# Kernel tuning notes

Measured on AMD Instinct MI355X. Metric: run time of the kernel, lower is better.

## Reference

```python
import jax, jax.numpy as jnp
import numpy as np

_CODESZ = 8   # E8 codeword dimension
_OFFSET = 0.25  # half-integer shift applied to D8 points


def _build_grid():
    # Faithful replication of get_grid(): cartesian product of arange(-4,4)
    # over 8 dims (torch.cartesian_prod order == 'ij' meshgrid, last dim fastest),
    # keep points with even coordinate sum and squared norm <= 10 (D8 subset),
    # then concat [d8 - 1/4, d8 + 1/4]. Yields 55650 codewords of dim 8.
    rng = np.arange(-4, 4, dtype=np.int8)
    pts = np.stack(np.meshgrid(*([rng] * _CODESZ), indexing='ij'), axis=-1).reshape(-1, _CODESZ)
    s = pts.sum(axis=-1, dtype=np.int16)
    n2 = (pts.astype(np.int16) * pts).sum(axis=-1)  # max 8*16 fits int16
    d8 = pts[(s % 2 == 0) & (n2 <= 10)].astype(np.float32)  # [27825, 8]
    grid = np.concatenate([d8 - _OFFSET, d8 + _OFFSET], axis=0)  # [55650, 8]
    grid_norm = (grid * grid).sum(axis=-1)  # diag(grid @ grid.T), [55650]
    return jnp.asarray(grid), jnp.asarray(grid_norm)


def setup_inputs() -> dict:
    key = jax.random.key(0)
    X = jax.random.normal(key, (8192, _CODESZ), dtype=jnp.float32)
    grid, grid_norm = _build_grid()
    return {"X": X, "grid": grid, "grid_norm": grid_norm}


def reference(X, grid, grid_norm):
    # quantize(X, return_idx=True):
    # nearest codeword under L2 <=> argmax of 2*X@g - ||g||^2
    scores = 2.0 * (X @ grid.T) - grid_norm          # [N, 55650]
    idx = jnp.argmax(scores, axis=-1)                # [N]
    vals = jnp.take(grid, idx, axis=0)               # [N, 8]
    idx_i16 = (idx + (-2 ** 15)).astype(jnp.int16)   # idx_offset + int16 cast
    return vals, idx_i16
```

## Files before the change

kernel.cpp:

```cpp
#include <hip/hip_runtime.h>
#include <math.h>


typedef short short8 __attribute__((ext_vector_type(8)));
typedef float f32x4  __attribute__((ext_vector_type(4)));

constexpr int NROWS  = 8192;
constexpr int NCW    = 55650;
constexpr int NT16   = 3488;
constexpr int NG     = 436;
constexpr int NCWP2  = NT16 * 16;
constexpr int NCHUNK = 32;
constexpr int RBLK   = 32;

constexpr size_t OFF_GB = 0;
constexpr size_t OFF_XS = OFF_GB + (size_t)NCWP2 * 32;
constexpr size_t OFF_BK = OFF_XS + (size_t)NROWS * 64;

__device__ inline unsigned short bf16_rne(float f) {
  unsigned int u = __float_as_uint(f);
  unsigned int r = u + 0x7FFFu + ((u >> 16) & 1u);
  return (unsigned short)(r >> 16);
}
__device__ inline float bf16_f(unsigned short h) {
  return __uint_as_float(((unsigned int)h) << 16);
}
__device__ inline unsigned int enc_ord(float f) {
  unsigned int u = __float_as_uint(f);
  return (u & 0x80000000u) ? ~u : (u | 0x80000000u);
}
__device__ inline float dec_ord(unsigned int e) {
  unsigned int u = (e & 0x80000000u) ? (e & 0x7FFFFFFFu) : ~e;
  return __uint_as_float(u);
}

__global__ __launch_bounds__(256) void e8_prep(
    const float* __restrict__ X, const float* __restrict__ G,
    const float* __restrict__ GN, unsigned short* __restrict__ Gb,
    unsigned short* __restrict__ Xs, unsigned long long* __restrict__ best) {
  int i = blockIdx.x * 256 + threadIdx.x;
  if (i < NCWP2) {
    unsigned short g16[16];
    if (i < NCW) {
      for (int j = 0; j < 8; ++j) g16[j] = bf16_rne(G[(size_t)i*8+j]);
      g16[8] = bf16_rne(GN[i]);
      for (int j = 9; j < 16; ++j) g16[j] = 0;
    } else {
      for (int j = 0; j < 8; ++j) g16[j] = 0;
      g16[8] = 0x7F7F;
      for (int j = 9; j < 16; ++j) g16[j] = 0;
    }
    uint4* dst = reinterpret_cast<uint4*>(Gb + (size_t)i * 16);
    dst[0] = *reinterpret_cast<uint4*>(&g16[0]);
    dst[1] = *reinterpret_cast<uint4*>(&g16[8]);
  } else if (i < NCWP2 + NROWS) {
    int r = i - NCWP2;
    unsigned short hh[8], mm[8], ll[8], qq[8];
    for (int j = 0; j < 8; ++j) {
      float s = 2.0f * X[(size_t)r*8+j];
      unsigned short h = bf16_rne(s);  float r1 = s  - bf16_f(h);
      unsigned short m = bf16_rne(r1); float r2 = r1 - bf16_f(m);
      unsigned short l = bf16_rne(r2);
      hh[j] = h; mm[j] = m; ll[j] = l;
      qq[j] = (j == 0) ? (unsigned short)0xBF80 : 0;
    }
    uint4* dst = reinterpret_cast<uint4*>(Xs + (size_t)r * 32);
    dst[0] = *reinterpret_cast<uint4*>(hh);
    dst[1] = *reinterpret_cast<uint4*>(mm);
    dst[2] = *reinterpret_cast<uint4*>(ll);
    dst[3] = *reinterpret_cast<uint4*>(qq);
    best[r] = 0ull;
  }
}

#define MV(d, s) "v_mov_b32 v" #d ", v" #s "\n\t"
#define MX(d, s) "v_max_f32 v" #d ", v" #d ", v" #s "\n\t"

#define T16A \
  "s_waitcnt vmcnt(1)\n\t" \
  "v_mfma_f32_16x16x32_bf16 v[72:75],  v[44:47], v[56:59], v[52:55]\n\t" \
  "v_mfma_f32_16x16x32_bf16 v[76:79],  v[44:47], v[60:63], v[52:55]\n\t" \
  "v_mfma_f32_16x16x32_bf16 v[80:83],  v[44:47], v[64:67], v[52:55]\n\t" \
  "v_mfma_f32_16x16x32_bf16 v[84:87],  v[44:47], v[68:71], v[52:55]\n\t" \
  "global_load_dwordx4 v[44:47], v40, %[gb]\n\t" \
  "v_add_u32 v40, 0x200, v40\n\t"

#define T16B \
  "s_waitcnt vmcnt(1)\n\t" \
  "v_mfma_f32_16x16x32_bf16 v[88:91],   v[48:51], v[56:59], v[52:55]\n\t" \
  "v_mfma_f32_16x16x32_bf16 v[92:95],   v[48:51], v[60:63], v[52:55]\n\t" \
  "v_mfma_f32_16x16x32_bf16 v[96:99],   v[48:51], v[64:67], v[52:55]\n\t" \
  "v_mfma_f32_16x16x32_bf16 v[100:103], v[48:51], v[68:71], v[52:55]\n\t" \
  "global_load_dwordx4 v[48:51], v40, %[gb]\n\t" \
  "v_add_u32 v40, 0x200, v40\n\t"

#define MOV16 \
  MV(104,72) MV(105,73) MV(106,74) MV(107,75) MV(108,76) MV(109,77) \
  MV(110,78) MV(111,79) MV(112,80) MV(113,81) MV(114,82) MV(115,83) \
  MV(116,84) MV(117,85) MV(118,86) MV(119,87)

#define MAXA16 \
  MX(104,72) MX(105,73) MX(106,74) MX(107,75) MX(108,76) MX(109,77) \
  MX(110,78) MX(111,79) MX(112,80) MX(113,81) MX(114,82) MX(115,83) \
  MX(116,84) MX(117,85) MX(118,86) MX(119,87)

#define MAXB16 \
  MX(104,88)  MX(105,89)  MX(106,90)  MX(107,91)  MX(108,92)  MX(109,93) \
  MX(110,94)  MX(111,95)  MX(112,96)  MX(113,97)  MX(114,98)  MX(115,99) \
  MX(116,100) MX(117,101) MX(118,102) MX(119,103)

#define TREETRACK \
  MX(104,105) MX(106,107) MX(108,109) MX(110,111) \
  MX(112,113) MX(114,115) MX(116,117) MX(118,119) \
  MX(104,106) MX(108,110) MX(112,114) MX(116,118) \
  "v_cmp_gt_f32 vcc, v104, v120\n\t" \
  "v_cndmask_b32 v124, v124, %[gi], vcc\n\t" \
  "v_max_f32 v120, v120, v104\n\t" \
  "v_cmp_gt_f32 vcc, v108, v121\n\t" \
  "v_cndmask_b32 v125, v125, %[gi], vcc\n\t" \
  "v_max_f32 v121, v121, v108\n\t" \
  "v_cmp_gt_f32 vcc, v112, v122\n\t" \
  "v_cndmask_b32 v126, v126, %[gi], vcc\n\t" \
  "v_max_f32 v122, v122, v112\n\t" \
  "v_cmp_gt_f32 vcc, v116, v123\n\t" \
  "v_cndmask_b32 v127, v127, %[gi], vcc\n\t" \
  "v_max_f32 v123, v123, v116\n\t"

#define GROUP16 \
  T16A T16B MOV16 T16A MAXB16 T16B MAXA16 \
  T16A MAXB16 T16B MAXA16 T16A MAXB16 T16B MAXA16 \
  "s_nop 7\n\t" "s_nop 7\n\t" MAXB16 TREETRACK "s_nop 0"

#define CLOBS \
  "v40","v41","v42","v43","v44","v45","v46","v47","v48","v49", \
  "v50","v51","v52","v53","v54","v55","v56","v57","v58","v59", \
  "v60","v61","v62","v63","v64","v65","v66","v67","v68","v69", \
  "v70","v71","v72","v73","v74","v75","v76","v77","v78","v79", \
  "v80","v81","v82","v83","v84","v85","v86","v87","v88","v89", \
  "v90","v91","v92","v93","v94","v95","v96","v97","v98","v99", \
  "v100","v101","v102","v103","v104","v105","v106","v107","v108","v109", \
  "v110","v111","v112","v113","v114","v115","v116","v117","v118","v119", \
  "v120","v121","v122","v123","v124","v125","v126","v127"

__global__ __launch_bounds__(256, 4) void e8_main(
    const unsigned short* __restrict__ Gb,
    const unsigned short* __restrict__ Xs,
    unsigned long long* __restrict__ best) {
  const int lane = threadIdx.x & 63;
  const int wave = threadIdx.x >> 6;
  const int l15 = lane & 15, kg = lane >> 4;
  const int rowbase = blockIdx.x * 256 + wave * 64;

  const int g0 = blockIdx.y * NG / NCHUNK;
  const int g1 = (blockIdx.y + 1) * NG / NCHUNK;
  const unsigned long long gbv = (unsigned long long)Gb;
  const unsigned long long xsv = (unsigned long long)Xs;

  unsigned avo = (unsigned)g0 * 4096u + (unsigned)l15 * 32u +
                 (kg == 3 ? 16u : 0u);
  unsigned bvo = (unsigned)(rowbase + l15) * 64u + (unsigned)kg * 16u;

  asm volatile(
      "v_mov_b32 v40, %[ao]\n\t"
      "v_mov_b32 v52, 0\n\t" "v_mov_b32 v53, 0\n\t"
      "v_mov_b32 v54, 0\n\t" "v_mov_b32 v55, 0\n\t"
      "v_mov_b32 v120, 0xff800000\n\t" "v_mov_b32 v121, 0xff800000\n\t"
      "v_mov_b32 v122, 0xff800000\n\t" "v_mov_b32 v123, 0xff800000\n\t"
      "v_mov_b32 v124, 0\n\t" "v_mov_b32 v125, 0\n\t"
      "v_mov_b32 v126, 0\n\t" "v_mov_b32 v127, 0\n\t"
      "global_load_dwordx4 v[56:59], %[bo], %[xs]\n\t"
      "global_load_dwordx4 v[60:63], %[bo], %[xs] offset:1024\n\t"
      "global_load_dwordx4 v[64:67], %[bo], %[xs] offset:2048\n\t"
      "global_load_dwordx4 v[68:71], %[bo], %[xs] offset:3072\n\t"
      "global_load_dwordx4 v[44:47], v40, %[gb]\n\t"
      "v_add_u32 v40, 0x200, v40\n\t"
      "global_load_dwordx4 v[48:51], v40, %[gb]\n\t"
      "v_add_u32 v40, 0x200, v40\n\t"
      "s_waitcnt vmcnt(0)"
      :: [gb]"s"(gbv), [xs]"s"(xsv), [ao]"v"(avo), [bo]"v"(bvo)
      : CLOBS, "memory");

  for (int g = g0; g < g1; ++g) {
    asm volatile(GROUP16
        :: [gb]"s"(gbv), [gi]"v"(g)
        : CLOBS, "vcc", "memory");
  }

  float bs0, bs1, bs2, bs3; int bi0, bi1, bi2, bi3;
  asm volatile(
      "s_waitcnt vmcnt(0)\n\t"
      "v_mov_b32 %0, v120\n\t" "v_mov_b32 %1, v121\n\t"
      "v_mov_b32 %2, v122\n\t" "v_mov_b32 %3, v123\n\t"
      "v_mov_b32 %4, v124\n\t" "v_mov_b32 %5, v125\n\t"
      "v_mov_b32 %6, v126\n\t" "v_mov_b32 %7, v127"
      : "=v"(bs0), "=v"(bs1), "=v"(bs2), "=v"(bs3),
        "=v"(bi0), "=v"(bi1), "=v"(bi2), "=v"(bi3) :: "memory");

  const float bsa[4] = {bs0, bs1, bs2, bs3};
  const int   bia[4] = {bi0, bi1, bi2, bi3};
#pragma unroll
  for (int t = 0; t < 4; ++t) {
    unsigned long long key =
        ((unsigned long long)enc_ord(bsa[t]) << 32) | (unsigned int)(~bia[t]);
    unsigned long long o = __shfl_xor(key, 16, 64);
    key = (o > key) ? o : key;
    o = __shfl_xor(key, 32, 64);
    key = (o > key) ? o : key;
    if (lane < 16)
      atomicMax(&best[(size_t)rowbase + t * 16 + l15], key);
  }
}

__global__ __launch_bounds__(256) void e8_resolve(
    const unsigned short* __restrict__ Gb,
    const unsigned short* __restrict__ Xs, const float* __restrict__ G,
    const unsigned long long* __restrict__ best, float* __restrict__ out) {
  const int lane = threadIdx.x & 63;
  const int wave = threadIdx.x >> 6;
  const int l15 = lane & 15, kg = lane >> 4;
  const int rt = blockIdx.x;

  short8 b;
  {
    const size_t row = (size_t)rt * 16 + l15;
    b = *reinterpret_cast<const short8*>(Xs + (row*4 + kg)*8);
  }
  f32x4 cz = {0.f, 0.f, 0.f, 0.f};

  for (int j = wave * 4; j < wave * 4 + 4; ++j) {
    const int srow = rt * 16 + j;
    const unsigned long long k = best[srow];
    const float sstar = dec_ord((unsigned int)(k >> 32));
    const int gwin = (int)(~(unsigned int)(k & 0xFFFFFFFFull));

    const int tb = gwin * 8;
    int cand = 0x7FFFFFFF;
    for (int tt = tb; tt < tb + 8; ++tt) {
      const unsigned short* ga =
          Gb + (size_t)tt * 256 + (size_t)l15 * 16 + (kg == 3 ? 8 : 0);
      short8 a = *reinterpret_cast<const short8*>(ga);
      f32x4 d = __builtin_amdgcn_mfma_f32_16x16x32_bf16(a, b, cz, 0, 0, 0);

      int tc = 0x0FFFFFFF;
#pragma unroll
      for (int r = 3; r >= 0; --r)
        tc = (d[r] == sstar) ? r : tc;
      const int gidx = tt * 16 + kg * 4 + tc;
      cand = (gidx < cand) ? gidx : cand;
    }
    if (l15 != j) cand = 0x7FFFFFFF;
    int o = __shfl_xor(cand, 16, 64); cand = min(cand, o);
    o = __shfl_xor(cand, 32, 64);     cand = min(cand, o);
    if (lane == j) {
      const float4* g = reinterpret_cast<const float4*>(G + (size_t)cand * 8);
      float4 v0 = g[0], v1 = g[1];
      float4* od = reinterpret_cast<float4*>(out + (size_t)srow * 8);
      od[0] = v0; od[1] = v1;
      out[(size_t)NROWS * 8 + srow] = (float)(cand - 32768);
    }
  }
}

extern "C" void kernel_launch(void* const* d_in, const int* in_sizes, int n_in,
                              void* d_out, int out_size, void* d_ws, size_t ws_size,
                              hipStream_t stream) {
  const float* X  = (const float*)d_in[0];
  const float* G  = (const float*)d_in[1];
  const float* GN = (const float*)d_in[2];
  float* out = (float*)d_out;

  char* ws = (char*)d_ws;
  unsigned short*     Gb   = (unsigned short*)(ws + OFF_GB);
  unsigned short*     Xs   = (unsigned short*)(ws + OFF_XS);
  unsigned long long* best = (unsigned long long*)(ws + OFF_BK);

  e8_prep<<<(NCWP2 + NROWS + 255) / 256, 256, 0, stream>>>(X, G, GN, Gb, Xs, best);
  e8_main<<<dim3(RBLK, NCHUNK), 256, 0, stream>>>(Gb, Xs, best);
  e8_resolve<<<512, 256, 0, stream>>>(Gb, Xs, G, best, out);
}
```

Measured before the change: 45.00 us.

## Stage codeword tiles in LDS with double buffering and fp32 norm accumulator init

Codeword tiles are repacked into 320-byte blocks holding 16 bf16 codewords plus their negated fp32 norms. Each group of 8 tiles is staged cooperatively into a double-buffered LDS region and read with ds_read_b128. The negated norm now enters as the MFMA accumulator input instead of an extra bf16 K-lane, so the norm subtraction is done in fp32 rather than bf16. This is meant to cut redundant per-wave global loads and use LDS reuse across the four waves. In exchange it adds a block barrier per group and changes the score rounding used by argmax.

```diff
diff --git a/kernel.cpp b/kernel.cpp
--- a/kernel.cpp
+++ b/kernel.cpp
@@ -4,6 +4,7 @@
 
 typedef short short8 __attribute__((ext_vector_type(8)));
 typedef float f32x4  __attribute__((ext_vector_type(4)));
+typedef unsigned int u32x4 __attribute__((ext_vector_type(4)));
 
 constexpr int NROWS  = 8192;
 constexpr int NCW    = 55650;
@@ -14,7 +15,7 @@
 constexpr int RBLK   = 32;
 
 constexpr size_t OFF_GB = 0;
-constexpr size_t OFF_XS = OFF_GB + (size_t)NCWP2 * 32;
+constexpr size_t OFF_XS = OFF_GB + (size_t)NT16 * 320;
 constexpr size_t OFF_BK = OFF_XS + (size_t)NROWS * 64;
 
 __device__ inline unsigned short bf16_rne(float f) {
@@ -36,23 +37,23 @@
 
 __global__ __launch_bounds__(256) void e8_prep(
     const float* __restrict__ X, const float* __restrict__ G,
-    const float* __restrict__ GN, unsigned short* __restrict__ Gb,
+    const float* __restrict__ GN, unsigned char* __restrict__ GbB,
     unsigned short* __restrict__ Xs, unsigned long long* __restrict__ best) {
   int i = blockIdx.x * 256 + threadIdx.x;
   if (i < NCWP2) {
-    unsigned short g16[16];
+    unsigned char* gt = GbB + (size_t)(i >> 4) * 320;
+    unsigned short c8[8];
+    float cgn;
     if (i < NCW) {
-      for (int j = 0; j < 8; ++j) g16[j] = bf16_rne(G[(size_t)i*8+j]);
-      g16[8] = bf16_rne(GN[i]);
-      for (int j = 9; j < 16; ++j) g16[j] = 0;
+      for (int j = 0; j < 8; ++j) c8[j] = bf16_rne(G[(size_t)i*8+j]);
+      cgn = -GN[i];
     } else {
-      for (int j = 0; j < 8; ++j) g16[j] = 0;
-      g16[8] = 0x7F7F;
-      for (int j = 9; j < 16; ++j) g16[j] = 0;
-    }
-    uint4* dst = reinterpret_cast<uint4*>(Gb + (size_t)i * 16);
-    dst[0] = *reinterpret_cast<uint4*>(&g16[0]);
-    dst[1] = *reinterpret_cast<uint4*>(&g16[8]);
+      for (int j = 0; j < 8; ++j) c8[j] = 0;
+      cgn = -3.0e38f;
+    }
+    *reinterpret_cast<u32x4*>(gt + (size_t)(i & 15) * 16) =
+        *reinterpret_cast<u32x4*>(c8);
+    *reinterpret_cast<float*>(gt + 256 + (size_t)(i & 15) * 4) = cgn;
   } else if (i < NCWP2 + NROWS) {
     int r = i - NCWP2;
     unsigned short hh[8], mm[8], ll[8], qq[8];
@@ -61,14 +62,13 @@
       unsigned short h = bf16_rne(s);  float r1 = s  - bf16_f(h);
       unsigned short m = bf16_rne(r1); float r2 = r1 - bf16_f(m);
       unsigned short l = bf16_rne(r2);
-      hh[j] = h; mm[j] = m; ll[j] = l;
-      qq[j] = (j == 0) ? (unsigned short)0xBF80 : 0;
-    }
-    uint4* dst = reinterpret_cast<uint4*>(Xs + (size_t)r * 32);
-    dst[0] = *reinterpret_cast<uint4*>(hh);
-    dst[1] = *reinterpret_cast<uint4*>(mm);
-    dst[2] = *reinterpret_cast<uint4*>(ll);
-    dst[3] = *reinterpret_cast<uint4*>(qq);
+      hh[j] = h; mm[j] = m; ll[j] = l; qq[j] = 0;
+    }
+    u32x4* dst = reinterpret_cast<u32x4*>(Xs + (size_t)r * 32);
+    dst[0] = *reinterpret_cast<u32x4*>(hh);
+    dst[1] = *reinterpret_cast<u32x4*>(mm);
+    dst[2] = *reinterpret_cast<u32x4*>(ll);
+    dst[3] = *reinterpret_cast<u32x4*>(qq);
     best[r] = 0ull;
   }
 }
@@ -76,62 +76,74 @@
 #define MV(d, s) "v_mov_b32 v" #d ", v" #s "\n\t"
 #define MX(d, s) "v_max_f32 v" #d ", v" #d ", v" #s "\n\t"
 
-#define T16A \
-  "s_waitcnt vmcnt(1)\n\t" \
-  "v_mfma_f32_16x16x32_bf16 v[72:75],  v[44:47], v[56:59], v[52:55]\n\t" \
-  "v_mfma_f32_16x16x32_bf16 v[76:79],  v[44:47], v[60:63], v[52:55]\n\t" \
-  "v_mfma_f32_16x16x32_bf16 v[80:83],  v[44:47], v[64:67], v[52:55]\n\t" \
-  "v_mfma_f32_16x16x32_bf16 v[84:87],  v[44:47], v[68:71], v[52:55]\n\t" \
-  "global_load_dwordx4 v[44:47], v40, %[gb]\n\t" \
-  "v_add_u32 v40, 0x200, v40\n\t"
-
-#define T16B \
-  "s_waitcnt vmcnt(1)\n\t" \
-  "v_mfma_f32_16x16x32_bf16 v[88:91],   v[48:51], v[56:59], v[52:55]\n\t" \
-  "v_mfma_f32_16x16x32_bf16 v[92:95],   v[48:51], v[60:63], v[52:55]\n\t" \
-  "v_mfma_f32_16x16x32_bf16 v[96:99],   v[48:51], v[64:67], v[52:55]\n\t" \
-  "v_mfma_f32_16x16x32_bf16 v[100:103], v[48:51], v[68:71], v[52:55]\n\t" \
-  "global_load_dwordx4 v[48:51], v40, %[gb]\n\t" \
-  "v_add_u32 v40, 0x200, v40\n\t"
+#define TE(P) \
+  "s_waitcnt lgkmcnt(2)\n\t" \
+  "v_mfma_f32_16x16x32_bf16 v[76:79], v[44:47], v[60:63], v[52:55]\n\t" \
+  "v_mfma_f32_16x16x32_bf16 v[80:83], v[44:47], v[64:67], v[52:55]\n\t" \
+  "v_mfma_f32_16x16x32_bf16 v[84:87], v[44:47], v[68:71], v[52:55]\n\t" \
+  "v_mfma_f32_16x16x32_bf16 v[88:91], v[44:47], v[72:75], v[52:55]\n\t" \
+  "ds_read_b128 v[44:47], v40 offset:" P "\n\t" \
+  "ds_read_b128 v[52:55], v41 offset:" P "\n\t"
+
+#define TO(P) \
+  "s_waitcnt lgkmcnt(2)\n\t" \
+  "v_mfma_f32_16x16x32_bf16 v[92:95],   v[48:51], v[60:63], v[56:59]\n\t" \
+  "v_mfma_f32_16x16x32_bf16 v[96:99],   v[48:51], v[64:67], v[56:59]\n\t" \
+  "v_mfma_f32_16x16x32_bf16 v[100:103], v[48:51], v[68:71], v[56:59]\n\t" \
+  "v_mfma_f32_16x16x32_bf16 v[104:107], v[48:51], v[72:75], v[56:59]\n\t" \
+  "ds_read_b128 v[48:51], v40 offset:" P "\n\t" \
+  "ds_read_b128 v[56:59], v41 offset:" P "\n\t"
 
 #define MOV16 \
-  MV(104,72) MV(105,73) MV(106,74) MV(107,75) MV(108,76) MV(109,77) \
-  MV(110,78) MV(111,79) MV(112,80) MV(113,81) MV(114,82) MV(115,83) \
-  MV(116,84) MV(117,85) MV(118,86) MV(119,87)
+  MV(108,76) MV(109,77) MV(110,78) MV(111,79) MV(112,80) MV(113,81) \
+  MV(114,82) MV(115,83) MV(116,84) MV(117,85) MV(118,86) MV(119,87) \
+  MV(120,88) MV(121,89) MV(122,90) MV(123,91)
 
 #define MAXA16 \
-  MX(104,72) MX(105,73) MX(106,74) MX(107,75) MX(108,76) MX(109,77) \
-  MX(110,78) MX(111,79) MX(112,80) MX(113,81) MX(114,82) MX(115,83) \
-  MX(116,84) MX(117,85) MX(118,86) MX(119,87)
+  MX(108,76) MX(109,77) MX(110,78) MX(111,79) MX(112,80) MX(113,81) \
+  MX(114,82) MX(115,83) MX(116,84) MX(117,85) MX(118,86) MX(119,87) \
+  MX(120,88) MX(121,89) MX(122,90) MX(123,91)
 
 #define MAXB16 \
-  MX(104,88)  MX(105,89)  MX(106,90)  MX(107,91)  MX(108,92)  MX(109,93) \
-  MX(110,94)  MX(111,95)  MX(112,96)  MX(113,97)  MX(114,98)  MX(115,99) \
-  MX(116,100) MX(117,101) MX(118,102) MX(119,103)
-
-#define TREETRACK \
-  MX(104,105) MX(106,107) MX(108,109) MX(110,111) \
-  MX(112,113) MX(114,115) MX(116,117) MX(118,119) \
-  MX(104,106) MX(108,110) MX(112,114) MX(116,118) \
-  "v_cmp_gt_f32 vcc, v104, v120\n\t" \
-  "v_cndmask_b32 v124, v124, %[gi], vcc\n\t" \
-  "v_max_f32 v120, v120, v104\n\t" \
-  "v_cmp_gt_f32 vcc, v108, v121\n\t" \
-  "v_cndmask_b32 v125, v125, %[gi], vcc\n\t" \
-  "v_max_f32 v121, v121, v108\n\t" \
-  "v_cmp_gt_f32 vcc, v112, v122\n\t" \
-  "v_cndmask_b32 v126, v126, %[gi], vcc\n\t" \
-  "v_max_f32 v122, v122, v112\n\t" \
-  "v_cmp_gt_f32 vcc, v116, v123\n\t" \
-  "v_cndmask_b32 v127, v127, %[gi], vcc\n\t" \
-  "v_max_f32 v123, v123, v116\n\t"
-
-#define GROUP16 \
-  T16A T16B MOV16 T16A MAXB16 T16B MAXA16 \
-  T16A MAXB16 T16B MAXA16 T16A MAXB16 T16B MAXA16 \
-  "s_nop 7\n\t" "s_nop 7\n\t" MAXB16 TREETRACK "s_nop 0"
+  MX(108,92)  MX(109,93)  MX(110,94)  MX(111,95)  MX(112,96)  MX(113,97) \
+  MX(114,98)  MX(115,99)  MX(116,100) MX(117,101) MX(118,102) MX(119,103) \
+  MX(120,104) MX(121,105) MX(122,106) MX(123,107)
+
+#define TREE \
+  MX(108,109) MX(110,111) MX(112,113) MX(114,115) \
+  MX(116,117) MX(118,119) MX(120,121) MX(122,123) \
+  MX(108,110) MX(112,114) MX(116,118) MX(120,122)
+
+#define TRACK \
+  "v_cmp_gt_f32 vcc, v108, v24\n\t" \
+  "v_cndmask_b32 v28, v28, %[gi], vcc\n\t" \
+  "v_max_f32 v24, v24, v108\n\t" \
+  "v_cmp_gt_f32 vcc, v112, v25\n\t" \
+  "v_cndmask_b32 v29, v29, %[gi], vcc\n\t" \
+  "v_max_f32 v25, v25, v112\n\t" \
+  "v_cmp_gt_f32 vcc, v116, v26\n\t" \
+  "v_cndmask_b32 v30, v30, %[gi], vcc\n\t" \
+  "v_max_f32 v26, v26, v116\n\t" \
+  "v_cmp_gt_f32 vcc, v120, v27\n\t" \
+  "v_cndmask_b32 v31, v31, %[gi], vcc\n\t" \
+  "v_max_f32 v27, v27, v120\n\t"
+
+#define BATCH8 \
+  "v_mov_b32 v40, %[la]\n\t" \
+  "v_mov_b32 v41, %[lc]\n\t" \
+  "ds_read_b128 v[44:47], v40\n\t" \
+  "ds_read_b128 v[52:55], v41\n\t" \
+  "ds_read_b128 v[48:51], v40 offset:320\n\t" \
+  "ds_read_b128 v[56:59], v41 offset:320\n\t" \
+  TE("640") TO("960") MOV16 \
+  TE("1280") MAXB16 TO("1600") MAXA16 \
+  TE("1920") MAXB16 TO("2240") MAXA16 \
+  TE("2560") MAXB16 TO("2880") MAXA16 \
+  "s_nop 7\n\t" "s_nop 7\n\t" \
+  MAXB16 TREE TRACK "s_nop 0"
 
 #define CLOBS \
+  "v24","v25","v26","v27","v28","v29","v30","v31", \
   "v40","v41","v42","v43","v44","v45","v46","v47","v48","v49", \
   "v50","v51","v52","v53","v54","v55","v56","v57","v58","v59", \
   "v60","v61","v62","v63","v64","v65","v66","v67","v68","v69", \
@@ -140,59 +152,87 @@
   "v90","v91","v92","v93","v94","v95","v96","v97","v98","v99", \
   "v100","v101","v102","v103","v104","v105","v106","v107","v108","v109", \
   "v110","v111","v112","v113","v114","v115","v116","v117","v118","v119", \
-  "v120","v121","v122","v123","v124","v125","v126","v127"
+  "v120","v121","v122","v123"
 
 __global__ __launch_bounds__(256, 4) void e8_main(
-    const unsigned short* __restrict__ Gb,
+    const unsigned char* __restrict__ GbB,
     const unsigned short* __restrict__ Xs,
     unsigned long long* __restrict__ best) {
-  const int lane = threadIdx.x & 63;
-  const int wave = threadIdx.x >> 6;
+  const int tid  = threadIdx.x;
+  const int lane = tid & 63;
+  const int wave = tid >> 6;
   const int l15 = lane & 15, kg = lane >> 4;
   const int rowbase = blockIdx.x * 256 + wave * 64;
 
+  __shared__ char smem[6912];
+  ((volatile char*)smem)[tid] = 0;
+
   const int g0 = blockIdx.y * NG / NCHUNK;
   const int g1 = (blockIdx.y + 1) * NG / NCHUNK;
-  const unsigned long long gbv = (unsigned long long)Gb;
   const unsigned long long xsv = (unsigned long long)Xs;
 
-  unsigned avo = (unsigned)g0 * 4096u + (unsigned)l15 * 32u +
-                 (kg == 3 ? 16u : 0u);
-  unsigned bvo = (unsigned)(rowbase + l15) * 64u + (unsigned)kg * 16u;
+  const unsigned bvo = (unsigned)(rowbase + l15) * 64u + (unsigned)kg * 16u;
 
   asm volatile(
-      "v_mov_b32 v40, %[ao]\n\t"
-      "v_mov_b32 v52, 0\n\t" "v_mov_b32 v53, 0\n\t"
-      "v_mov_b32 v54, 0\n\t" "v_mov_b32 v55, 0\n\t"
-      "v_mov_b32 v120, 0xff800000\n\t" "v_mov_b32 v121, 0xff800000\n\t"
-      "v_mov_b32 v122, 0xff800000\n\t" "v_mov_b32 v123, 0xff800000\n\t"
-      "v_mov_b32 v124, 0\n\t" "v_mov_b32 v125, 0\n\t"
-      "v_mov_b32 v126, 0\n\t" "v_mov_b32 v127, 0\n\t"
-      "global_load_dwordx4 v[56:59], %[bo], %[xs]\n\t"
-      "global_load_dwordx4 v[60:63], %[bo], %[xs] offset:1024\n\t"
-      "global_load_dwordx4 v[64:67], %[bo], %[xs] offset:2048\n\t"
-      "global_load_dwordx4 v[68:71], %[bo], %[xs] offset:3072\n\t"
-      "global_load_dwordx4 v[44:47], v40, %[gb]\n\t"
-      "v_add_u32 v40, 0x200, v40\n\t"
-      "global_load_dwordx4 v[48:51], v40, %[gb]\n\t"
-      "v_add_u32 v40, 0x200, v40\n\t"
+      "v_mov_b32 v24, 0xff800000\n\t" "v_mov_b32 v25, 0xff800000\n\t"
+      "v_mov_b32 v26, 0xff800000\n\t" "v_mov_b32 v27, 0xff800000\n\t"
+      "v_mov_b32 v28, 0\n\t" "v_mov_b32 v29, 0\n\t"
+      "v_mov_b32 v30, 0\n\t" "v_mov_b32 v31, 0\n\t"
+      "global_load_dwordx4 v[60:63], %[bo], %[xs]\n\t"
+      "global_load_dwordx4 v[64:67], %[bo], %[xs] offset:1024\n\t"
+      "global_load_dwordx4 v[68:71], %[bo], %[xs] offset:2048\n\t"
+      "global_load_dwordx4 v[72:75], %[bo], %[xs] offset:3072\n\t"
       "s_waitcnt vmcnt(0)"
-      :: [gb]"s"(gbv), [xs]"s"(xsv), [ao]"v"(avo), [bo]"v"(bvo)
+      :: [xs]"s"(xsv), [bo]"v"(bvo)
       : CLOBS, "memory");
 
+  if (tid < 80) {
+    const u32x4* s = reinterpret_cast<const u32x4*>(
+        GbB + (size_t)g0 * 2560 + (size_t)tid * 32);
+    u32x4 a = s[0], b2 = s[1];
+    unsigned doff = (unsigned)tid * 32u;
+    asm volatile(
+        "ds_write_b128 %[ad], %[v0]\n\t"
+        "ds_write_b128 %[ad], %[v1] offset:16"
+        :: [ad]"v"(doff), [v0]"v"(a), [v1]"v"(b2) : "memory");
+  }
+  __syncthreads();
+
   for (int g = g0; g < g1; ++g) {
-    asm volatile(GROUP16
-        :: [gb]"s"(gbv), [gi]"v"(g)
+    const int gnx = g + 1;
+    const bool do_stage = (gnx < g1) && (tid < 80);
+    u32x4 va = {0,0,0,0}, vb2 = {0,0,0,0};
+    if (do_stage) {
+      const u32x4* s = reinterpret_cast<const u32x4*>(
+          GbB + (size_t)gnx * 2560 + (size_t)tid * 32);
+      va = s[0]; vb2 = s[1];
+    }
+
+    const unsigned par = (unsigned)((g - g0) & 1) * 3328u;
+    const unsigned la = par + (unsigned)l15 * 16u;
+    const unsigned lc = par + 256u + (unsigned)kg * 16u;
+    asm volatile(BATCH8
+        :: [la]"v"(la), [lc]"v"(lc), [gi]"v"(g)
         : CLOBS, "vcc", "memory");
+
+    if (do_stage) {
+      const unsigned doff =
+          (unsigned)((gnx - g0) & 1) * 3328u + (unsigned)tid * 32u;
+      asm volatile(
+          "ds_write_b128 %[ad], %[v0]\n\t"
+          "ds_write_b128 %[ad], %[v1] offset:16"
+          :: [ad]"v"(doff), [v0]"v"(va), [v1]"v"(vb2) : "memory");
+    }
+    __syncthreads();
   }
 
   float bs0, bs1, bs2, bs3; int bi0, bi1, bi2, bi3;
   asm volatile(
-      "s_waitcnt vmcnt(0)\n\t"
-      "v_mov_b32 %0, v120\n\t" "v_mov_b32 %1, v121\n\t"
-      "v_mov_b32 %2, v122\n\t" "v_mov_b32 %3, v123\n\t"
-      "v_mov_b32 %4, v124\n\t" "v_mov_b32 %5, v125\n\t"
-      "v_mov_b32 %6, v126\n\t" "v_mov_b32 %7, v127"
+      "s_waitcnt vmcnt(0) lgkmcnt(0)\n\t"
+      "v_mov_b32 %0, v24\n\t" "v_mov_b32 %1, v25\n\t"
+      "v_mov_b32 %2, v26\n\t" "v_mov_b32 %3, v27\n\t"
+      "v_mov_b32 %4, v28\n\t" "v_mov_b32 %5, v29\n\t"
+      "v_mov_b32 %6, v30\n\t" "v_mov_b32 %7, v31"
       : "=v"(bs0), "=v"(bs1), "=v"(bs2), "=v"(bs3),
         "=v"(bi0), "=v"(bi1), "=v"(bi2), "=v"(bi3) :: "memory");
 
@@ -212,7 +252,7 @@
 }
 
 __global__ __launch_bounds__(256) void e8_resolve(
-    const unsigned short* __restrict__ Gb,
+    const unsigned char* __restrict__ GbB,
     const unsigned short* __restrict__ Xs, const float* __restrict__ G,
     const unsigned long long* __restrict__ best, float* __restrict__ out) {
   const int lane = threadIdx.x & 63;
@@ -225,7 +265,6 @@
     const size_t row = (size_t)rt * 16 + l15;
     b = *reinterpret_cast<const short8*>(Xs + (row*4 + kg)*8);
   }
-  f32x4 cz = {0.f, 0.f, 0.f, 0.f};
 
   for (int j = wave * 4; j < wave * 4 + 4; ++j) {
     const int srow = rt * 16 + j;
@@ -236,10 +275,10 @@
     const int tb = gwin * 8;
     int cand = 0x7FFFFFFF;
     for (int tt = tb; tt < tb + 8; ++tt) {
-      const unsigned short* ga =
-          Gb + (size_t)tt * 256 + (size_t)l15 * 16 + (kg == 3 ? 8 : 0);
-      short8 a = *reinterpret_cast<const short8*>(ga);
-      f32x4 d = __builtin_amdgcn_mfma_f32_16x16x32_bf16(a, b, cz, 0, 0, 0);
+      const unsigned char* gt = GbB + (size_t)tt * 320;
+      short8 a = *reinterpret_cast<const short8*>(gt + (size_t)l15 * 16);
+      f32x4 C = *reinterpret_cast<const f32x4*>(gt + 256 + (size_t)kg * 16);
+      f32x4 d = __builtin_amdgcn_mfma_f32_16x16x32_bf16(a, b, C, 0, 0, 0);
 
       int tc = 0x0FFFFFFF;
 #pragma unroll
@@ -270,11 +309,11 @@
   float* out = (float*)d_out;
 
   char* ws = (char*)d_ws;
-  unsigned short*     Gb   = (unsigned short*)(ws + OFF_GB);
+  unsigned char*      GbB  = (unsigned char*)(ws + OFF_GB);
   unsigned short*     Xs   = (unsigned short*)(ws + OFF_XS);
   unsigned long long* best = (unsigned long long*)(ws + OFF_BK);
 
-  e8_prep<<<(NCWP2 + NROWS + 255) / 256, 256, 0, stream>>>(X, G, GN, Gb, Xs, best);
-  e8_main<<<dim3(RBLK, NCHUNK), 256, 0, stream>>>(Gb, Xs, best);
-  e8_resolve<<<512, 256, 0, stream>>>(Gb, Xs, G, best, out);
-}
+  e8_prep<<<(NCWP2 + NROWS + 255) / 256, 256, 0, stream>>>(X, G, GN, GbB, Xs, best);
+  e8_main<<<dim3(RBLK, NCHUNK), 256, 0, stream>>>(GbB, Xs, best);
+  e8_resolve<<<512, 256, 0, stream>>>(GbB, Xs, G, best, out);
+}
```

After: 45.99 us. 2.2% more time.
